# Kernel optimization log

Hardware: AMD Instinct MI355X
Metric: run time of the kernel (lower is better)

Reference implementation:

```python
import jax, jax.numpy as jnp
import numpy as np

N = 20000      # nodes
E = 320000     # edges (avg degree 16)
D_IN = 128     # input_dim
HID = 128      # graph_hidden_dim (per-head channels)
HEADS = 4


def setup_inputs() -> dict:
    key = jax.random.key(0)
    ks = jax.random.split(key, 16)
    def gl(k, shape, fan_in):
        return jax.random.normal(k, shape, jnp.float32) / np.float32(np.sqrt(fan_in))
    x = jax.random.normal(ks[0], (N, D_IN), jnp.float32)
    edge_index = jax.random.randint(ks[1], (2, E), 0, N, dtype=jnp.int64)
    # layer 0: in=D_IN, heads=4, concat -> 4*HID
    W0 = gl(ks[2], (D_IN, HEADS * HID), D_IN)
    a_src0 = gl(ks[3], (HEADS, HID), HID)
    a_dst0 = gl(ks[4], (HEADS, HID), HID)
    b0 = jnp.zeros((HEADS * HID,), jnp.float32)
    # layer 1: in=4*HID, heads=4, concat -> 4*HID
    W1 = gl(ks[5], (HEADS * HID, HEADS * HID), HEADS * HID)
    a_src1 = gl(ks[6], (HEADS, HID), HID)
    a_dst1 = gl(ks[7], (HEADS, HID), HID)
    b1 = jnp.zeros((HEADS * HID,), jnp.float32)
    # layer 2: in=4*HID, heads=1, no concat -> HID
    W2 = gl(ks[8], (HEADS * HID, HID), HEADS * HID)
    a_src2 = gl(ks[9], (1, HID), HID)
    a_dst2 = gl(ks[10], (1, HID), HID)
    b2 = jnp.zeros((HID,), jnp.float32)
    # output MLP: HID -> HID//2 -> 1
    Wm1 = gl(ks[11], (HID, HID // 2), HID)
    bm1 = jnp.zeros((HID // 2,), jnp.float32)
    Wm2 = gl(ks[12], (HID // 2, 1), HID // 2)
    bm2 = jnp.zeros((1,), jnp.float32)
    return dict(x=x, edge_index=edge_index, W0=W0, a_src0=a_src0, a_dst0=a_dst0, b0=b0,
                W1=W1, a_src1=a_src1, a_dst1=a_dst1, b1=b1,
                W2=W2, a_src2=a_src2, a_dst2=a_dst2, b2=b2,
                Wm1=Wm1, bm1=bm1, Wm2=Wm2, bm2=bm2)


def _gat(x, src, dst, W, a_s, a_d, b, heads, ch, concat):
    """PyG GATConv: per-head linear, edge attention with LeakyReLU(0.2),
    segment softmax over incoming edges, scatter-add aggregation."""
    n = x.shape[0]
    xl = (x @ W).reshape(n, heads, ch)                      # [N,H,C]
    a_src_n = jnp.einsum('nhc,hc->nh', xl, a_s)             # [N,H]
    a_dst_n = jnp.einsum('nhc,hc->nh', xl, a_d)
    e = jax.nn.leaky_relu(a_src_n[src] + a_dst_n[dst], 0.2) # [E,H]
    m = jax.ops.segment_max(e, dst, num_segments=n)
    ex = jnp.exp(e - m[dst])
    den = jax.ops.segment_sum(ex, dst, num_segments=n)
    alpha = ex / den[dst]                                   # self-loops keep den > 0
    out = jax.ops.segment_sum(alpha[:, :, None] * xl[src], dst, num_segments=n)  # [N,H,C]
    out = out.reshape(n, heads * ch) if concat else out.mean(axis=1)
    return out + b


def reference(x, edge_index, W0, a_src0, a_dst0, b0, W1, a_src1, a_dst1, b1,
              W2, a_src2, a_dst2, b2, Wm1, bm1, Wm2, bm2):
    n = x.shape[0]
    loops = jnp.arange(n, dtype=edge_index.dtype)           # add_self_loops (PyG default)
    src = jnp.concatenate([edge_index[0], loops])
    dst = jnp.concatenate([edge_index[1], loops])
    h = jax.nn.relu(_gat(x, src, dst, W0, a_src0, a_dst0, b0, HEADS, HID, True))
    h = jax.nn.relu(_gat(h, src, dst, W1, a_src1, a_dst1, b1, HEADS, HID, True))
    h = _gat(h, src, dst, W2, a_src2, a_dst2, b2, 1, HID, False)
    g = h.mean(axis=0, keepdims=True)                       # global mean pool, batch=None -> [1,HID]
    g = jax.nn.relu(g @ Wm1 + bm1)
    return g @ Wm2 + bm2                                    # predictions [1,1]
```

## Files before the change

kernel.cpp:

```cpp
#include <hip/hip_runtime.h>
#include <math.h>


typedef float f32x4 __attribute__((ext_vector_type(4)));
typedef float f32x2 __attribute__((ext_vector_type(2)));
typedef short s16x8 __attribute__((ext_vector_type(8)));
typedef short s16x4 __attribute__((ext_vector_type(4)));

__device__ inline ushort f2bf(float f) {
  unsigned u = __float_as_uint(f);
  u += 0x7FFF + ((u >> 16) & 1);
  return (ushort)(u >> 16);
}
__device__ inline float bf2f(ushort h) { return __uint_as_float((unsigned)h << 16); }
__device__ inline unsigned char f2fp8(float f) {
  int p = __builtin_amdgcn_cvt_pk_fp8_f32(f, f, 0, false);
  return (unsigned char)(p & 0xFF);
}

__global__ void prep_kernel(
    const float* __restrict__ W0, const float* __restrict__ W1,
    const float* __restrict__ W2, ushort* __restrict__ w0h, ushort* __restrict__ w0l,
    ushort* __restrict__ w1h, ushort* __restrict__ w1l, ushort* __restrict__ w2h,
    ushort* __restrict__ w2l, const int* __restrict__ ei, int* __restrict__ counts,
    int E, int n) {
  int idx = blockIdx.x * 256 + threadIdx.x;
  if (idx >= 98304) {
    int t = idx - 98304;
    if (t < E)          atomicAdd(&counts[ei[E + t]], 1);
    else if (t < E + n) atomicAdd(&counts[t - E], 1);
    return;
  }
  const float* W; ushort *th, *tl; int K, N;
  if (idx < 16384)      { W = W0; th = w0h; tl = w0l; K = 128; N = 512; }
  else if (idx < 81920) { idx -= 16384; W = W1; th = w1h; tl = w1l; K = 512; N = 512; }
  else                  { idx -= 81920; W = W2; th = w2h; tl = w2l; K = 512; N = 128; }
  int nn = idx % N;
  int k4 = (idx / N) << 2;
  s16x4 hv, lv;
#pragma unroll
  for (int r = 0; r < 4; ++r) {
    float w = W[(size_t)(k4 + r) * N + nn];
    ushort h = f2bf(w);
    hv[r] = (short)h;
    lv[r] = (short)f2bf(w - bf2f(h));
  }
  *(s16x4*)&th[(size_t)nn * K + k4] = hv;
  *(s16x4*)&tl[(size_t)nn * K + k4] = lv;
}

__global__ void scan1_kernel(const int* __restrict__ counts, int* __restrict__ partials,
                             int n) {
  __shared__ int sd[4];
  int i = blockIdx.x * 256 + threadIdx.x;
  int v = (i < n) ? counts[i] : 0;
  for (int m = 32; m; m >>= 1) v += __shfl_xor(v, m);
  if ((threadIdx.x & 63) == 0) sd[threadIdx.x >> 6] = v;
  __syncthreads();
  if (threadIdx.x == 0) partials[blockIdx.x] = sd[0] + sd[1] + sd[2] + sd[3];
}

__global__ void scan3_kernel(const int* __restrict__ counts, const int* __restrict__ partials,
                             int* __restrict__ offsets, int n) {
  __shared__ int sd[256];
  __shared__ int cw[4];
  __shared__ int carry_sh;
  int t = threadIdx.x;
  int pv = (t < blockIdx.x) ? partials[t] : 0;
  for (int m = 32; m; m >>= 1) pv += __shfl_xor(pv, m);
  if ((t & 63) == 0) cw[t >> 6] = pv;
  __syncthreads();
  if (t == 0) carry_sh = cw[0] + cw[1] + cw[2] + cw[3];
  int i = blockIdx.x * 256 + t;
  int v = (i < n) ? counts[i] : 0;
  sd[t] = v;
  __syncthreads();
  for (int off = 1; off < 256; off <<= 1) {
    int u = (t >= off) ? sd[t - off] : 0;
    __syncthreads();
    sd[t] += u;
    __syncthreads();
  }
  int carry = carry_sh;
  if (i < n) {
    offsets[i] = carry + sd[t] - v;
    if (i == n - 1) offsets[n] = carry + sd[t];
  }
}

__global__ void scatter_kernel(const int* __restrict__ ei, const int* __restrict__ offsets,
                               int* __restrict__ cursor, int* __restrict__ srcs,
                               int E, int n) {
  int t = blockIdx.x * blockDim.x + threadIdx.x;
  int s, d;
  if (t < E)          { s = ei[t]; d = ei[E + t]; }
  else if (t < E + n) { s = t - E; d = s; }
  else return;
  int pos = offsets[d] + atomicAdd(&cursor[d], 1);
  srcs[pos] = s;
}

template <int NC>
__device__ inline void gemm_epilogue(
    f32x4 (&acc)[2][4], unsigned char* __restrict__ Cb, const float* __restrict__ a_s,
    const float* __restrict__ a_d, float* __restrict__ asn, float* __restrict__ adn,
    float (*st_sh)[64][2], int M, int row0, int col0, int hidx,
    int tid, int lane, int wid, int wm, int wn, int fr) {
  constexpr int N = NC * 128;
  float asv[4], adv[4];
#pragma unroll
  for (int j = 0; j < 4; ++j) {
    asv[j] = a_s[hidx * 128 + wn + j * 16 + fr];
    adv[j] = a_d[hidx * 128 + wn + j * 16 + fr];
  }
  int rb = row0 + wm + ((lane >> 4) << 2);
  int cb = col0 + wn + fr;
#pragma unroll
  for (int i = 0; i < 2; ++i)
#pragma unroll
    for (int r = 0; r < 4; ++r) {
      int row = rb + i * 16 + r;
      float sp = 0.f, dp = 0.f;
#pragma unroll
      for (int j = 0; j < 4; ++j) {
        float c = acc[i][j][r];
        sp += c * asv[j];
        dp += c * adv[j];
        if (row < M) Cb[(size_t)row * N + cb + j * 16] = f2fp8(c);
      }
#pragma unroll
      for (int m = 1; m < 16; m <<= 1) {
        sp += __shfl_xor(sp, m);
        dp += __shfl_xor(dp, m);
      }
      if ((lane & 15) == 0) {
        int rowb = wm + i * 16 + ((lane >> 4) << 2) + r;
        st_sh[0][rowb][wid >> 1] = sp;
        st_sh[1][rowb][wid >> 1] = dp;
      }
    }
  __syncthreads();
  if (tid < 64) {
    int row = row0 + tid;
    if (row < M) {
      asn[(size_t)row * NC + hidx] = st_sh[0][tid][0] + st_sh[0][tid][1];
      adn[(size_t)row * NC + hidx] = st_sh[1][tid][0] + st_sh[1][tid][1];
    }
  }
}

template <int NC>
__global__ __launch_bounds__(256, 2) void gemm_f32a_kernel(
    const float* __restrict__ A, const ushort* __restrict__ Bth,
    const ushort* __restrict__ Btl, unsigned char* __restrict__ Cb,
    const float* __restrict__ a_s, const float* __restrict__ a_d,
    float* __restrict__ asn, float* __restrict__ adn,
    int M, int K) {
  __shared__ s16x8 Ash[4][64], Asl[4][64];
  __shared__ s16x8 Bsh[4][128], Bsl[4][128];
  __shared__ float st_sh[2][64][2];
  int id = blockIdx.x;
  int rs = (id / (8 * NC)) * 8 + (id & 7);
  int row0 = rs * 64;
  if (row0 >= M) return;
  int hidx = (id >> 3) % NC;
  int col0 = hidx * 128;
  int tid = threadIdx.x;
  int am = tid >> 2, aq = tid & 3;
  int bn = tid >> 1, bq = (tid & 1) << 1;
  int lane = tid & 63, wid = tid >> 6;
  int wm = (wid & 1) << 5, wn = (wid >> 1) << 6;
  int fr = lane & 15, fqq = lane >> 4;
  f32x4 acc[2][4] = {};
  const float* Arow = A + (size_t)(row0 + am) * K + aq * 8;
  bool avalid = (row0 + am) < M;
  const ushort* bhp = Bth + (size_t)(col0 + bn) * K + bq * 8;
  const ushort* blp = Btl + (size_t)(col0 + bn) * K + bq * 8;

  for (int k0 = 0; k0 < K; k0 += 32) {
    float v[8];
    if (avalid) {
      float4 t0 = *(const float4*)(Arow + k0);
      float4 t1 = *(const float4*)(Arow + k0 + 4);
      v[0] = t0.x; v[1] = t0.y; v[2] = t0.z; v[3] = t0.w;
      v[4] = t1.x; v[5] = t1.y; v[6] = t1.z; v[7] = t1.w;
    } else {
#pragma unroll
      for (int r = 0; r < 8; ++r) v[r] = 0.f;
    }
    s16x8 hv, lv;
#pragma unroll
    for (int r = 0; r < 8; ++r) {
      ushort h = f2bf(v[r]);
      hv[r] = (short)h;
      lv[r] = (short)f2bf(v[r] - bf2f(h));
    }
    Ash[aq][am] = hv;
    Asl[aq][am] = lv;
    Bsh[bq][bn]     = *(const s16x8*)(bhp + k0);
    Bsh[bq + 1][bn] = *(const s16x8*)(bhp + k0 + 8);
    Bsl[bq][bn]     = *(const s16x8*)(blp + k0);
    Bsl[bq + 1][bn] = *(const s16x8*)(blp + k0 + 8);
    __syncthreads();
    s16x8 ah[2], al[2], bh[4], bl[4];
#pragma unroll
    for (int i = 0; i < 2; ++i) {
      ah[i] = Ash[fqq][wm + i * 16 + fr];
      al[i] = Asl[fqq][wm + i * 16 + fr];
    }
#pragma unroll
    for (int j = 0; j < 4; ++j) {
      bh[j] = Bsh[fqq][wn + j * 16 + fr];
      bl[j] = Bsl[fqq][wn + j * 16 + fr];
    }
#pragma unroll
    for (int i = 0; i < 2; ++i)
#pragma unroll
      for (int j = 0; j < 4; ++j) {
        acc[i][j] = __builtin_amdgcn_mfma_f32_16x16x32_bf16(ah[i], bh[j], acc[i][j], 0, 0, 0);
        acc[i][j] = __builtin_amdgcn_mfma_f32_16x16x32_bf16(ah[i], bl[j], acc[i][j], 0, 0, 0);
        acc[i][j] = __builtin_amdgcn_mfma_f32_16x16x32_bf16(al[i], bh[j], acc[i][j], 0, 0, 0);
      }
    __syncthreads();
  }
  gemm_epilogue<NC>(acc, Cb, a_s, a_d, asn, adn, st_sh, M, row0, col0, hidx,
                    tid, lane, wid, wm, wn, fr);
}

template <int NC>
__global__ __launch_bounds__(256, 2) void gemm_bf16a_kernel(
    const ushort* __restrict__ A, const ushort* __restrict__ Bth,
    const ushort* __restrict__ Btl, unsigned char* __restrict__ Cb,
    const float* __restrict__ a_s, const float* __restrict__ a_d,
    float* __restrict__ asn, float* __restrict__ adn,
    int M, int K) {
  __shared__ s16x8 Ash[4][64];
  __shared__ s16x8 Bsh[4][128], Bsl[4][128];
  __shared__ float st_sh[2][64][2];
  int id = blockIdx.x;
  int rs = (id / (8 * NC)) * 8 + (id & 7);
  int row0 = rs * 64;
  if (row0 >= M) return;
  int hidx = (id >> 3) % NC;
  int col0 = hidx * 128;
  int tid = threadIdx.x;
  int am = tid >> 2, aq = tid & 3;
  int bn = tid >> 1, bq = (tid & 1) << 1;
  int lane = tid & 63, wid = tid >> 6;
  int wm = (wid & 1) << 5, wn = (wid >> 1) << 6;
  int fr = lane & 15, fqq = lane >> 4;
  f32x4 acc[2][4] = {};
  const ushort* Arow = A + (size_t)(row0 + am) * K + aq * 8;
  bool avalid = (row0 + am) < M;
  const ushort* bhp = Bth + (size_t)(col0 + bn) * K + bq * 8;
  const ushort* blp = Btl + (size_t)(col0 + bn) * K + bq * 8;
  const s16x8 zero8 = {};

  for (int k0 = 0; k0 < K; k0 += 32) {
    Ash[aq][am] = avalid ? *(const s16x8*)(Arow + k0) : zero8;
    Bsh[bq][bn]     = *(const s16x8*)(bhp + k0);
    Bsh[bq + 1][bn] = *(const s16x8*)(bhp + k0 + 8);
    Bsl[bq][bn]     = *(const s16x8*)(blp + k0);
    Bsl[bq + 1][bn] = *(const s16x8*)(blp + k0 + 8);
    __syncthreads();
    s16x8 ah[2], bh[4], bl[4];
#pragma unroll
    for (int i = 0; i < 2; ++i) ah[i] = Ash[fqq][wm + i * 16 + fr];
#pragma unroll
    for (int j = 0; j < 4; ++j) {
      bh[j] = Bsh[fqq][wn + j * 16 + fr];
      bl[j] = Bsl[fqq][wn + j * 16 + fr];
    }
#pragma unroll
    for (int i = 0; i < 2; ++i)
#pragma unroll
      for (int j = 0; j < 4; ++j) {
        acc[i][j] = __builtin_amdgcn_mfma_f32_16x16x32_bf16(ah[i], bh[j], acc[i][j], 0, 0, 0);
        acc[i][j] = __builtin_amdgcn_mfma_f32_16x16x32_bf16(ah[i], bl[j], acc[i][j], 0, 0, 0);
      }
    __syncthreads();
  }
  gemm_epilogue<NC>(acc, Cb, a_s, a_d, asn, adn, st_sh, M, row0, col0, hidx,
                    tid, lane, wid, wm, wn, fr);
}

template <int NC>
__global__ __launch_bounds__(256, 2) void gemm_bf16a128_kernel(
    const ushort* __restrict__ A, const ushort* __restrict__ Bth,
    const ushort* __restrict__ Btl, unsigned char* __restrict__ Cb,
    const float* __restrict__ a_s, const float* __restrict__ a_d,
    float* __restrict__ asn, float* __restrict__ adn,
    int M, int K) {
  constexpr int N = NC * 128;
  __shared__ s16x8 Ash[4][128];
  __shared__ s16x8 Bsh[4][128], Bsl[4][128];
  __shared__ float st_sh[2][128][2];
  int id = blockIdx.x;
  int rs = (id / (8 * NC)) * 8 + (id & 7);
  int row0 = rs * 128;
  if (row0 >= M) return;
  int hidx = (id >> 3) % NC;
  int col0 = hidx * 128;
  int tid = threadIdx.x;
  int am = tid >> 1, aq = (tid & 1) << 1;
  int bn = tid >> 1, bq = (tid & 1) << 1;
  int lane = tid & 63, wid = tid >> 6;
  int wm = (wid & 1) << 6, wn = (wid >> 1) << 6;
  int fr = lane & 15, fqq = lane >> 4;
  f32x4 acc[4][4] = {};
  const ushort* Arow = A + (size_t)(row0 + am) * K + aq * 8;
  bool avalid = (row0 + am) < M;
  const ushort* bhp = Bth + (size_t)(col0 + bn) * K + bq * 8;
  const ushort* blp = Btl + (size_t)(col0 + bn) * K + bq * 8;
  const s16x8 zero8 = {};

  for (int k0 = 0; k0 < K; k0 += 32) {
    Ash[aq][am]     = avalid ? *(const s16x8*)(Arow + k0) : zero8;
    Ash[aq + 1][am] = avalid ? *(const s16x8*)(Arow + k0 + 8) : zero8;
    Bsh[bq][bn]     = *(const s16x8*)(bhp + k0);
    Bsh[bq + 1][bn] = *(const s16x8*)(bhp + k0 + 8);
    Bsl[bq][bn]     = *(const s16x8*)(blp + k0);
    Bsl[bq + 1][bn] = *(const s16x8*)(blp + k0 + 8);
    __syncthreads();
    s16x8 ah[4], bh[4], bl[4];
#pragma unroll
    for (int i = 0; i < 4; ++i) ah[i] = Ash[fqq][wm + i * 16 + fr];
#pragma unroll
    for (int j = 0; j < 4; ++j) {
      bh[j] = Bsh[fqq][wn + j * 16 + fr];
      bl[j] = Bsl[fqq][wn + j * 16 + fr];
    }
#pragma unroll
    for (int i = 0; i < 4; ++i)
#pragma unroll
      for (int j = 0; j < 4; ++j) {
        acc[i][j] = __builtin_amdgcn_mfma_f32_16x16x32_bf16(ah[i], bh[j], acc[i][j], 0, 0, 0);
        acc[i][j] = __builtin_amdgcn_mfma_f32_16x16x32_bf16(ah[i], bl[j], acc[i][j], 0, 0, 0);
      }
    __syncthreads();
  }
  float asv[4], adv[4];
#pragma unroll
  for (int j = 0; j < 4; ++j) {
    asv[j] = a_s[hidx * 128 + wn + j * 16 + fr];
    adv[j] = a_d[hidx * 128 + wn + j * 16 + fr];
  }
  int rb = row0 + wm + ((lane >> 4) << 2);
  int cb = col0 + wn + fr;
#pragma unroll
  for (int i = 0; i < 4; ++i)
#pragma unroll
    for (int r = 0; r < 4; ++r) {
      int row = rb + i * 16 + r;
      float sp = 0.f, dp = 0.f;
#pragma unroll
      for (int j = 0; j < 4; ++j) {
        float c = acc[i][j][r];
        sp += c * asv[j];
        dp += c * adv[j];
        if (row < M) Cb[(size_t)row * N + cb + j * 16] = f2fp8(c);
      }
#pragma unroll
      for (int m = 1; m < 16; m <<= 1) {
        sp += __shfl_xor(sp, m);
        dp += __shfl_xor(dp, m);
      }
      if ((lane & 15) == 0) {
        int rowb = wm + i * 16 + ((lane >> 4) << 2) + r;
        st_sh[0][rowb][wid >> 1] = sp;
        st_sh[1][rowb][wid >> 1] = dp;
      }
    }
  __syncthreads();
  if (tid < 128) {
    int row = row0 + tid;
    if (row < M) {
      asn[(size_t)row * NC + hidx] = st_sh[0][tid][0] + st_sh[0][tid][1];
      adn[(size_t)row * NC + hidx] = st_sh[1][tid][0] + st_sh[1][tid][1];
    }
  }
}

__global__ __launch_bounds__(256) void agg4_kernel(
    const unsigned char* __restrict__ xl, const float* __restrict__ asn,
    const float* __restrict__ adn, const int* __restrict__ offsets,
    const int* __restrict__ srcs, const float* __restrict__ bias,
    ushort* __restrict__ out, int n) {
  __shared__ float alpha_sh[4][4][64];
  __shared__ int src_sh[4][64];
  int wib = threadIdx.x >> 6, lane = threadIdx.x & 63;
  int nd = blockIdx.x * 4 + wib;
  if (nd >= n) return;
  int beg = offsets[nd], deg = offsets[nd + 1] - beg;
  float4 adl = *(const float4*)&adn[(size_t)nd * 4];
  int ch0 = lane << 3;
  int hm = lane >> 4;
  float den[4] = {0.f, 0.f, 0.f, 0.f};
  float acc[8] = {};

  for (int j0 = 0; j0 < deg; j0 += 64) {
    int j = j0 + lane;
    int s = 0;
    float w0 = 0.f, w1 = 0.f, w2 = 0.f, w3 = 0.f;
    if (j < deg) {
      s = srcs[beg + j];
      float4 av = *(const float4*)&asn[(size_t)s * 4];
      float e;
      e = av.x + adl.x; e = (e > 0.f) ? e : 0.2f * e; w0 = __expf(fminf(e, 30.f));
      e = av.y + adl.y; e = (e > 0.f) ? e : 0.2f * e; w1 = __expf(fminf(e, 30.f));
      e = av.z + adl.z; e = (e > 0.f) ? e : 0.2f * e; w2 = __expf(fminf(e, 30.f));
      e = av.w + adl.w; e = (e > 0.f) ? e : 0.2f * e; w3 = __expf(fminf(e, 30.f));
      den[0] += w0; den[1] += w1; den[2] += w2; den[3] += w3;
    }
    src_sh[wib][lane] = s;
    alpha_sh[wib][0][lane] = w0;
    alpha_sh[wib][1][lane] = w1;
    alpha_sh[wib][2][lane] = w2;
    alpha_sh[wib][3][lane] = w3;
    __builtin_amdgcn_wave_barrier();
    int cl = min(64, deg - j0);
    int jj = 0;
    for (; jj + 8 <= cl; jj += 8) {
      int4 sv0 = *(const int4*)&src_sh[wib][jj];
      int4 sv1 = *(const int4*)&src_sh[wib][jj + 4];
      float4 av0 = *(const float4*)&alpha_sh[wib][hm][jj];
      float4 av1 = *(const float4*)&alpha_sh[wib][hm][jj + 4];
      uint2 v[8];
      v[0] = *(const uint2*)(xl + (size_t)sv0.x * 512 + ch0);
      v[1] = *(const uint2*)(xl + (size_t)sv0.y * 512 + ch0);
      v[2] = *(const uint2*)(xl + (size_t)sv0.z * 512 + ch0);
      v[3] = *(const uint2*)(xl + (size_t)sv0.w * 512 + ch0);
      v[4] = *(const uint2*)(xl + (size_t)sv1.x * 512 + ch0);
      v[5] = *(const uint2*)(xl + (size_t)sv1.y * 512 + ch0);
      v[6] = *(const uint2*)(xl + (size_t)sv1.z * 512 + ch0);
      v[7] = *(const uint2*)(xl + (size_t)sv1.w * 512 + ch0);
      float a[8] = {av0.x, av0.y, av0.z, av0.w, av1.x, av1.y, av1.z, av1.w};
#pragma unroll
      for (int u = 0; u < 8; ++u) {
        f32x2 c01 = __builtin_amdgcn_cvt_pk_f32_fp8((int)v[u].x, false);
        f32x2 c23 = __builtin_amdgcn_cvt_pk_f32_fp8((int)v[u].x, true);
        f32x2 c45 = __builtin_amdgcn_cvt_pk_f32_fp8((int)v[u].y, false);
        f32x2 c67 = __builtin_amdgcn_cvt_pk_f32_fp8((int)v[u].y, true);
        acc[0] += a[u] * c01[0]; acc[1] += a[u] * c01[1];
        acc[2] += a[u] * c23[0]; acc[3] += a[u] * c23[1];
        acc[4] += a[u] * c45[0]; acc[5] += a[u] * c45[1];
        acc[6] += a[u] * c67[0]; acc[7] += a[u] * c67[1];
      }
    }
    for (; jj < cl; ++jj) {
      int s2 = src_sh[wib][jj];
      float a = alpha_sh[wib][hm][jj];
      uint2 v = *(const uint2*)(xl + (size_t)s2 * 512 + ch0);
      f32x2 c01 = __builtin_amdgcn_cvt_pk_f32_fp8((int)v.x, false);
      f32x2 c23 = __builtin_amdgcn_cvt_pk_f32_fp8((int)v.x, true);
      f32x2 c45 = __builtin_amdgcn_cvt_pk_f32_fp8((int)v.y, false);
      f32x2 c67 = __builtin_amdgcn_cvt_pk_f32_fp8((int)v.y, true);
      acc[0] += a * c01[0]; acc[1] += a * c01[1];
      acc[2] += a * c23[0]; acc[3] += a * c23[1];
      acc[4] += a * c45[0]; acc[5] += a * c45[1];
      acc[6] += a * c67[0]; acc[7] += a * c67[1];
    }
    __builtin_amdgcn_wave_barrier();
  }
#pragma unroll
  for (int h = 0; h < 4; ++h)
    for (int m = 1; m < 64; m <<= 1) den[h] += __shfl_xor(den[h], m);
  float d = (hm == 0) ? den[0] : (hm == 1) ? den[1] : (hm == 2) ? den[2] : den[3];
  float inv = 1.f / d;
  s16x8 ob;
#pragma unroll
  for (int i = 0; i < 8; ++i)
    ob[i] = (short)f2bf(fmaxf(acc[i] * inv + bias[ch0 + i], 0.f));
  *(s16x8*)(out + (size_t)nd * 512 + ch0) = ob;
}

__global__ __launch_bounds__(256) void agg1_pool_kernel(
    const unsigned char* __restrict__ xl, const float* __restrict__ asn,
    const float* __restrict__ adn, const int* __restrict__ offsets,
    const int* __restrict__ srcs, const float* __restrict__ bias,
    float* __restrict__ g_part, int n) {
  __shared__ float alpha_sh[4][64];
  __shared__ int src_sh[4][64];
  __shared__ float red_sh[4][128];
  int wib = threadIdx.x >> 6, lane = threadIdx.x & 63;
  int nd = blockIdx.x * 4 + wib;
  bool valid = nd < n;
  int ch0 = lane << 1;
  float acc0 = 0.f, acc1 = 0.f;

  if (valid) {
    int beg = offsets[nd], deg = offsets[nd + 1] - beg;
    float adl = adn[nd];
    float den = 0.f;
    for (int j0 = 0; j0 < deg; j0 += 64) {
      int j = j0 + lane;
      int s = 0;
      float w = 0.f;
      if (j < deg) {
        s = srcs[beg + j];
        float e = asn[s] + adl;
        e = (e > 0.f) ? e : 0.2f * e;
        w = __expf(fminf(e, 30.f));
        den += w;
      }
      src_sh[wib][lane] = s;
      alpha_sh[wib][lane] = w;
      __builtin_amdgcn_wave_barrier();
      int cl = min(64, deg - j0);
      int jj = 0;
      for (; jj + 4 <= cl; jj += 4) {
        int4 sv = *(const int4*)&src_sh[wib][jj];
        float4 av = *(const float4*)&alpha_sh[wib][jj];
        uint v0 = *(const ushort*)(xl + (size_t)sv.x * 128 + ch0);
        uint v1 = *(const ushort*)(xl + (size_t)sv.y * 128 + ch0);
        uint v2 = *(const ushort*)(xl + (size_t)sv.z * 128 + ch0);
        uint v3 = *(const ushort*)(xl + (size_t)sv.w * 128 + ch0);
        f32x2 c0 = __builtin_amdgcn_cvt_pk_f32_fp8((int)v0, false);
        f32x2 c1 = __builtin_amdgcn_cvt_pk_f32_fp8((int)v1, false);
        f32x2 c2 = __builtin_amdgcn_cvt_pk_f32_fp8((int)v2, false);
        f32x2 c3 = __builtin_amdgcn_cvt_pk_f32_fp8((int)v3, false);
        acc0 += av.x * c0[0]; acc1 += av.x * c0[1];
        acc0 += av.y * c1[0]; acc1 += av.y * c1[1];
        acc0 += av.z * c2[0]; acc1 += av.z * c2[1];
        acc0 += av.w * c3[0]; acc1 += av.w * c3[1];
      }
      for (; jj < cl; ++jj) {
        int s2 = src_sh[wib][jj];
        float a = alpha_sh[wib][jj];
        uint v = *(const ushort*)(xl + (size_t)s2 * 128 + ch0);
        f32x2 c = __builtin_amdgcn_cvt_pk_f32_fp8((int)v, false);
        acc0 += a * c[0]; acc1 += a * c[1];
      }
      __builtin_amdgcn_wave_barrier();
    }
    for (int m = 1; m < 64; m <<= 1) den += __shfl_xor(den, m);
    float inv = 1.f / den;
    acc0 = acc0 * inv + bias[ch0 + 0];
    acc1 = acc1 * inv + bias[ch0 + 1];
  }
  red_sh[wib][ch0] = acc0;
  red_sh[wib][ch0 + 1] = acc1;
  __syncthreads();
  if (threadIdx.x < 128) {
    float s = red_sh[0][threadIdx.x] + red_sh[1][threadIdx.x] +
              red_sh[2][threadIdx.x] + red_sh[3][threadIdx.x];
    atomicAdd(&g_part[(blockIdx.x & 63) * 128 + threadIdx.x], s);
  }
}

__global__ void mlp_kernel(const float* __restrict__ g_part,
                           const float* __restrict__ Wm1, const float* __restrict__ bm1,
                           const float* __restrict__ Wm2, const float* __restrict__ bm2,
                           float* __restrict__ out, float invn) {
  __shared__ float gs[128];
  __shared__ float hs[64];
  int t = threadIdx.x;
  float s = 0.f;
  for (int k = 0; k < 64; ++k) s += g_part[k * 128 + t];
  gs[t] = s * invn;
  __syncthreads();
  if (t < 64) {
    float acc = bm1[t];
    for (int c = 0; c < 128; ++c) acc += gs[c] * Wm1[c * 64 + t];
    hs[t] = fmaxf(acc, 0.f);
  }
  __syncthreads();
  if (t == 0) {
    float o = bm2[0];
    for (int j = 0; j < 64; ++j) o += hs[j] * Wm2[j];
    out[0] = o;
  }
}

extern "C" void kernel_launch(void* const* d_in, const int* in_sizes, int n_in,
                              void* d_out, int out_size, void* d_ws, size_t ws_size,
                              hipStream_t stream) {
  const float* x   = (const float*)d_in[0];
  const int*   ei  = (const int*)d_in[1];
  const float* W0  = (const float*)d_in[2];
  const float* as0 = (const float*)d_in[3];
  const float* ad0 = (const float*)d_in[4];
  const float* b0  = (const float*)d_in[5];
  const float* W1  = (const float*)d_in[6];
  const float* as1 = (const float*)d_in[7];
  const float* ad1 = (const float*)d_in[8];
  const float* b1  = (const float*)d_in[9];
  const float* W2  = (const float*)d_in[10];
  const float* as2 = (const float*)d_in[11];
  const float* ad2 = (const float*)d_in[12];
  const float* b2  = (const float*)d_in[13];
  const float* Wm1 = (const float*)d_in[14];
  const float* bm1 = (const float*)d_in[15];
  const float* Wm2 = (const float*)d_in[16];
  const float* bm2 = (const float*)d_in[17];

  const int N = in_sizes[0] / 128;
  const int E = in_sizes[1] / 2;
  const int ET = E + N;

  ushort* hb  = (ushort*)d_ws;
  unsigned char* xlb = (unsigned char*)(hb + (size_t)N * 512);
  float*  asn = (float*)(xlb + (size_t)N * 512);
  float*  adn = asn + (size_t)N * 4;
  float*  gp  = adn + (size_t)N * 4;
  int* counts = (int*)(gp + 64 * 128);
  int* cursor = counts + N;
  int* offs   = cursor + N;
  int* srcs   = offs + N + 1;
  int* parts  = srcs + ET;
  ushort* w0h = (ushort*)(((uintptr_t)(parts + 1024) + 63) & ~(uintptr_t)63);
  ushort* w0l = w0h + 512 * 128;
  ushort* w1h = w0l + 512 * 128;
  ushort* w1l = w1h + 512 * 512;
  ushort* w2h = w1l + 512 * 512;
  ushort* w2l = w2h + 128 * 512;

  hipMemsetAsync(gp, 0, (size_t)(64 * 128 + 2 * N) * sizeof(int), stream);

  prep_kernel<<<(98304 + ET + 255) / 256, 256, 0, stream>>>(
      W0, W1, W2, w0h, w0l, w1h, w1l, w2h, w2l, ei, counts, E, N);

  int ebl = (ET + 255) / 256;
  int nb = (N + 255) / 256;
  scan1_kernel<<<nb, 256, 0, stream>>>(counts, parts, N);
  scan3_kernel<<<nb, 256, 0, stream>>>(counts, parts, offs, N);
  scatter_kernel<<<ebl, 256, 0, stream>>>(ei, offs, cursor, srcs, E, N);

  int nwb4 = (N + 3) / 4;
  int rsn = (N + 63) / 64;
  int rsp = ((rsn + 7) / 8) * 8;
  int blk0 = rsp * 4;
  int rs128 = (N + 127) / 128;
  int rsp128 = ((rs128 + 7) / 8) * 8;
  int blk1 = rsp128 * 4;
  int blk2 = rsp;

  gemm_f32a_kernel<4><<<blk0, 256, 0, stream>>>(x, w0h, w0l, xlb, as0, ad0,
                                                asn, adn, N, 128);
  agg4_kernel<<<nwb4, 256, 0, stream>>>(xlb, asn, adn, offs, srcs, b0, hb, N);

  gemm_bf16a128_kernel<4><<<blk1, 256, 0, stream>>>(hb, w1h, w1l, xlb, as1, ad1,
                                                    asn, adn, N, 512);
  agg4_kernel<<<nwb4, 256, 0, stream>>>(xlb, asn, adn, offs, srcs, b1, hb, N);

  gemm_bf16a_kernel<1><<<blk2, 256, 0, stream>>>(hb, w2h, w2l, xlb, as2, ad2,
                                                 asn, adn, N, 512);
  agg1_pool_kernel<<<nwb4, 256, 0, stream>>>(xlb, asn, adn, offs, srcs, b2, gp, N);

  mlp_kernel<<<1, 128, 0, stream>>>(gp, Wm1, bm1, Wm2, bm2, (float*)d_out,
                                    1.0f / (float)N);
}
```

Measured before the change: 280.2 us.

## Fuse all pipeline stages into one cooperative persistent kernel with grid syncs

Replaces the sequence of separate launches (memset, prep, scan, scatter, three GEMMs, three aggregations, MLP) with one cooperative persistent kernel. Each stage loops over virtual block ids and is separated from the next by grid.sync(), with shared memory held in a union sized for the largest stage. This removes per-launch overhead and inter-kernel gaps. In exchange it adds grid-wide barrier costs, a launch bound of 3 blocks per CU that may limit registers for the GEMMs, and load imbalance where a stage has fewer blocks than the grid; the old multi-kernel path is kept as a fallback.

```diff
diff --git a/kernel.cpp b/kernel.cpp
--- a/kernel.cpp
+++ b/kernel.cpp
@@ -1,5 +1,8 @@
 #include <hip/hip_runtime.h>
+#include <hip/hip_cooperative_groups.h>
 #include <math.h>
+
+namespace cg = cooperative_groups;
 
 
 typedef float f32x4 __attribute__((ext_vector_type(4)));
@@ -18,13 +21,21 @@
   return (unsigned char)(p & 0xFF);
 }
 
-__global__ void prep_kernel(
-    const float* __restrict__ W0, const float* __restrict__ W1,
+struct SG0 { s16x8 Ash[4][64]; s16x8 Asl[4][64]; s16x8 Bsh[4][128]; s16x8 Bsl[4][128]; float st[2][64][2]; };
+struct SG1 { s16x8 Ash[4][128]; s16x8 Bsh[4][128]; s16x8 Bsl[4][128]; float st[2][128][2]; };
+struct SG2 { s16x8 Ash[4][64]; s16x8 Bsh[4][128]; s16x8 Bsl[4][128]; float st[2][64][2]; };
+struct SA4 { float alpha[4][4][64]; int src[4][64]; };
+struct SA1 { float alpha[4][64]; int src[4][64]; float red[4][128]; };
+struct SSCAN { int sd[256]; int cw[4]; int carry; };
+struct SMLP { float gs[128]; float hs[64]; };
+union SMem { SG0 g0; SG1 g1; SG2 g2; SA4 a4; SA1 a1; SSCAN scan; SMLP mlp; };
+
+__device__ inline void prep_item(
+    int idx, const float* __restrict__ W0, const float* __restrict__ W1,
     const float* __restrict__ W2, ushort* __restrict__ w0h, ushort* __restrict__ w0l,
     ushort* __restrict__ w1h, ushort* __restrict__ w1l, ushort* __restrict__ w2h,
     ushort* __restrict__ w2l, const int* __restrict__ ei, int* __restrict__ counts,
     int E, int n) {
-  int idx = blockIdx.x * 256 + threadIdx.x;
   if (idx >= 98304) {
     int t = idx - 98304;
     if (t < E)          atomicAdd(&counts[ei[E + t]], 1);
@@ -49,49 +60,49 @@
   *(s16x4*)&tl[(size_t)nn * K + k4] = lv;
 }
 
-__global__ void scan1_kernel(const int* __restrict__ counts, int* __restrict__ partials,
-                             int n) {
-  __shared__ int sd[4];
-  int i = blockIdx.x * 256 + threadIdx.x;
+__device__ inline void scan1_body(int vb, const int* __restrict__ counts,
+                                  int* __restrict__ partials, int n, SSCAN& s) {
+  int t = threadIdx.x;
+  int i = vb * 256 + t;
   int v = (i < n) ? counts[i] : 0;
   for (int m = 32; m; m >>= 1) v += __shfl_xor(v, m);
-  if ((threadIdx.x & 63) == 0) sd[threadIdx.x >> 6] = v;
-  __syncthreads();
-  if (threadIdx.x == 0) partials[blockIdx.x] = sd[0] + sd[1] + sd[2] + sd[3];
-}
-
-__global__ void scan3_kernel(const int* __restrict__ counts, const int* __restrict__ partials,
-                             int* __restrict__ offsets, int n) {
-  __shared__ int sd[256];
-  __shared__ int cw[4];
-  __shared__ int carry_sh;
+  if ((t & 63) == 0) s.cw[t >> 6] = v;
+  __syncthreads();
+  if (t == 0) partials[vb] = s.cw[0] + s.cw[1] + s.cw[2] + s.cw[3];
+  __syncthreads();
+}
+
+__device__ inline void scan3_body(int vb, const int* __restrict__ counts,
+                                  const int* __restrict__ partials,
+                                  int* __restrict__ offsets, int n, SSCAN& s) {
   int t = threadIdx.x;
-  int pv = (t < blockIdx.x) ? partials[t] : 0;
+  int pv = (t < vb) ? partials[t] : 0;
   for (int m = 32; m; m >>= 1) pv += __shfl_xor(pv, m);
-  if ((t & 63) == 0) cw[t >> 6] = pv;
-  __syncthreads();
-  if (t == 0) carry_sh = cw[0] + cw[1] + cw[2] + cw[3];
-  int i = blockIdx.x * 256 + t;
+  if ((t & 63) == 0) s.cw[t >> 6] = pv;
+  __syncthreads();
+  if (t == 0) s.carry = s.cw[0] + s.cw[1] + s.cw[2] + s.cw[3];
+  int i = vb * 256 + t;
   int v = (i < n) ? counts[i] : 0;
-  sd[t] = v;
+  s.sd[t] = v;
   __syncthreads();
   for (int off = 1; off < 256; off <<= 1) {
-    int u = (t >= off) ? sd[t - off] : 0;
+    int u = (t >= off) ? s.sd[t - off] : 0;
     __syncthreads();
-    sd[t] += u;
+    s.sd[t] += u;
     __syncthreads();
   }
-  int carry = carry_sh;
+  int carry = s.carry;
   if (i < n) {
-    offsets[i] = carry + sd[t] - v;
-    if (i == n - 1) offsets[n] = carry + sd[t];
-  }
-}
-
-__global__ void scatter_kernel(const int* __restrict__ ei, const int* __restrict__ offsets,
-                               int* __restrict__ cursor, int* __restrict__ srcs,
-                               int E, int n) {
-  int t = blockIdx.x * blockDim.x + threadIdx.x;
+    offsets[i] = carry + s.sd[t] - v;
+    if (i == n - 1) offsets[n] = carry + s.sd[t];
+  }
+  __syncthreads();
+}
+
+__device__ inline void scatter_item(int t, const int* __restrict__ ei,
+                                    const int* __restrict__ offsets,
+                                    int* __restrict__ cursor, int* __restrict__ srcs,
+                                    int E, int n) {
   int s, d;
   if (t < E)          { s = ei[t]; d = ei[E + t]; }
   else if (t < E + n) { s = t - E; d = s; }
@@ -150,16 +161,11 @@
 }
 
 template <int NC>
-__global__ __launch_bounds__(256, 2) void gemm_f32a_kernel(
-    const float* __restrict__ A, const ushort* __restrict__ Bth,
+__device__ inline void gemm_f32a_body(
+    int id, const float* __restrict__ A, const ushort* __restrict__ Bth,
     const ushort* __restrict__ Btl, unsigned char* __restrict__ Cb,
     const float* __restrict__ a_s, const float* __restrict__ a_d,
-    float* __restrict__ asn, float* __restrict__ adn,
-    int M, int K) {
-  __shared__ s16x8 Ash[4][64], Asl[4][64];
-  __shared__ s16x8 Bsh[4][128], Bsl[4][128];
-  __shared__ float st_sh[2][64][2];
-  int id = blockIdx.x;
+    float* __restrict__ asn, float* __restrict__ adn, int M, int K, SG0& sm) {
   int rs = (id / (8 * NC)) * 8 + (id & 7);
   int row0 = rs * 64;
   if (row0 >= M) return;
@@ -195,23 +201,23 @@
       hv[r] = (short)h;
       lv[r] = (short)f2bf(v[r] - bf2f(h));
     }
-    Ash[aq][am] = hv;
-    Asl[aq][am] = lv;
-    Bsh[bq][bn]     = *(const s16x8*)(bhp + k0);
-    Bsh[bq + 1][bn] = *(const s16x8*)(bhp + k0 + 8);
-    Bsl[bq][bn]     = *(const s16x8*)(blp + k0);
-    Bsl[bq + 1][bn] = *(const s16x8*)(blp + k0 + 8);
+    sm.Ash[aq][am] = hv;
+    sm.Asl[aq][am] = lv;
+    sm.Bsh[bq][bn]     = *(const s16x8*)(bhp + k0);
+    sm.Bsh[bq + 1][bn] = *(const s16x8*)(bhp + k0 + 8);
+    sm.Bsl[bq][bn]     = *(const s16x8*)(blp + k0);
+    sm.Bsl[bq + 1][bn] = *(const s16x8*)(blp + k0 + 8);
     __syncthreads();
     s16x8 ah[2], al[2], bh[4], bl[4];
 #pragma unroll
     for (int i = 0; i < 2; ++i) {
-      ah[i] = Ash[fqq][wm + i * 16 + fr];
-      al[i] = Asl[fqq][wm + i * 16 + fr];
+      ah[i] = sm.Ash[fqq][wm + i * 16 + fr];
+      al[i] = sm.Asl[fqq][wm + i * 16 + fr];
     }
 #pragma unroll
     for (int j = 0; j < 4; ++j) {
-      bh[j] = Bsh[fqq][wn + j * 16 + fr];
-      bl[j] = Bsl[fqq][wn + j * 16 + fr];
+      bh[j] = sm.Bsh[fqq][wn + j * 16 + fr];
+      bl[j] = sm.Bsl[fqq][wn + j * 16 + fr];
     }
 #pragma unroll
     for (int i = 0; i < 2; ++i)
@@ -223,21 +229,16 @@
       }
     __syncthreads();
   }
-  gemm_epilogue<NC>(acc, Cb, a_s, a_d, asn, adn, st_sh, M, row0, col0, hidx,
+  gemm_epilogue<NC>(acc, Cb, a_s, a_d, asn, adn, sm.st, M, row0, col0, hidx,
                     tid, lane, wid, wm, wn, fr);
 }
 
 template <int NC>
-__global__ __launch_bounds__(256, 2) void gemm_bf16a_kernel(
-    const ushort* __restrict__ A, const ushort* __restrict__ Bth,
+__device__ inline void gemm_bf16a_body(
+    int id, const ushort* __restrict__ A, const ushort* __restrict__ Bth,
     const ushort* __restrict__ Btl, unsigned char* __restrict__ Cb,
     const float* __restrict__ a_s, const float* __restrict__ a_d,
-    float* __restrict__ asn, float* __restrict__ adn,
-    int M, int K) {
-  __shared__ s16x8 Ash[4][64];
-  __shared__ s16x8 Bsh[4][128], Bsl[4][128];
-  __shared__ float st_sh[2][64][2];
-  int id = blockIdx.x;
+    float* __restrict__ asn, float* __restrict__ adn, int M, int K, SG2& sm) {
   int rs = (id / (8 * NC)) * 8 + (id & 7);
   int row0 = rs * 64;
   if (row0 >= M) return;
@@ -257,19 +258,19 @@
   const s16x8 zero8 = {};
 
   for (int k0 = 0; k0 < K; k0 += 32) {
-    Ash[aq][am] = avalid ? *(const s16x8*)(Arow + k0) : zero8;
-    Bsh[bq][bn]     = *(const s16x8*)(bhp + k0);
-    Bsh[bq + 1][bn] = *(const s16x8*)(bhp + k0 + 8);
-    Bsl[bq][bn]     = *(const s16x8*)(blp + k0);
-    Bsl[bq + 1][bn] = *(const s16x8*)(blp + k0 + 8);
+    sm.Ash[aq][am] = avalid ? *(const s16x8*)(Arow + k0) : zero8;
+    sm.Bsh[bq][bn]     = *(const s16x8*)(bhp + k0);
+    sm.Bsh[bq + 1][bn] = *(const s16x8*)(bhp + k0 + 8);
+    sm.Bsl[bq][bn]     = *(const s16x8*)(blp + k0);
+    sm.Bsl[bq + 1][bn] = *(const s16x8*)(blp + k0 + 8);
     __syncthreads();
     s16x8 ah[2], bh[4], bl[4];
 #pragma unroll
-    for (int i = 0; i < 2; ++i) ah[i] = Ash[fqq][wm + i * 16 + fr];
+    for (int i = 0; i < 2; ++i) ah[i] = sm.Ash[fqq][wm + i * 16 + fr];
 #pragma unroll
     for (int j = 0; j < 4; ++j) {
-      bh[j] = Bsh[fqq][wn + j * 16 + fr];
-      bl[j] = Bsl[fqq][wn + j * 16 + fr];
+      bh[j] = sm.Bsh[fqq][wn + j * 16 + fr];
+      bl[j] = sm.Bsl[fqq][wn + j * 16 + fr];
     }
 #pragma unroll
     for (int i = 0; i < 2; ++i)
@@ -280,22 +281,17 @@
       }
     __syncthreads();
   }
-  gemm_epilogue<NC>(acc, Cb, a_s, a_d, asn, adn, st_sh, M, row0, col0, hidx,
+  gemm_epilogue<NC>(acc, Cb, a_s, a_d, asn, adn, sm.st, M, row0, col0, hidx,
                     tid, lane, wid, wm, wn, fr);
 }
 
 template <int NC>
-__global__ __launch_bounds__(256, 2) void gemm_bf16a128_kernel(
-    const ushort* __restrict__ A, const ushort* __restrict__ Bth,
+__device__ inline void gemm_bf16a128_body(
+    int id, const ushort* __restrict__ A, const ushort* __restrict__ Bth,
     const ushort* __restrict__ Btl, unsigned char* __restrict__ Cb,
     const float* __restrict__ a_s, const float* __restrict__ a_d,
-    float* __restrict__ asn, float* __restrict__ adn,
-    int M, int K) {
+    float* __restrict__ asn, float* __restrict__ adn, int M, int K, SG1& sm) {
   constexpr int N = NC * 128;
-  __shared__ s16x8 Ash[4][128];
-  __shared__ s16x8 Bsh[4][128], Bsl[4][128];
-  __shared__ float st_sh[2][128][2];
-  int id = blockIdx.x;
   int rs = (id / (8 * NC)) * 8 + (id & 7);
   int row0 = rs * 128;
   if (row0 >= M) return;
@@ -315,20 +311,20 @@
   const s16x8 zero8 = {};
 
   for (int k0 = 0; k0 < K; k0 += 32) {
-    Ash[aq][am]     = avalid ? *(const s16x8*)(Arow + k0) : zero8;
-    Ash[aq + 1][am] = avalid ? *(const s16x8*)(Arow + k0 + 8) : zero8;
-    Bsh[bq][bn]     = *(const s16x8*)(bhp + k0);
-    Bsh[bq + 1][bn] = *(const s16x8*)(bhp + k0 + 8);
-    Bsl[bq][bn]     = *(const s16x8*)(blp + k0);
-    Bsl[bq + 1][bn] = *(const s16x8*)(blp + k0 + 8);
+    sm.Ash[aq][am]     = avalid ? *(const s16x8*)(Arow + k0) : zero8;
+    sm.Ash[aq + 1][am] = avalid ? *(const s16x8*)(Arow + k0 + 8) : zero8;
+    sm.Bsh[bq][bn]     = *(const s16x8*)(bhp + k0);
+    sm.Bsh[bq + 1][bn] = *(const s16x8*)(bhp + k0 + 8);
+    sm.Bsl[bq][bn]     = *(const s16x8*)(blp + k0);
+    sm.Bsl[bq + 1][bn] = *(const s16x8*)(blp + k0 + 8);
     __syncthreads();
     s16x8 ah[4], bh[4], bl[4];
 #pragma unroll
-    for (int i = 0; i < 4; ++i) ah[i] = Ash[fqq][wm + i * 16 + fr];
+    for (int i = 0; i < 4; ++i) ah[i] = sm.Ash[fqq][wm + i * 16 + fr];
 #pragma unroll
     for (int j = 0; j < 4; ++j) {
-      bh[j] = Bsh[fqq][wn + j * 16 + fr];
-      bl[j] = Bsl[fqq][wn + j * 16 + fr];
+      bh[j] = sm.Bsh[fqq][wn + j * 16 + fr];
+      bl[j] = sm.Bsl[fqq][wn + j * 16 + fr];
     }
 #pragma unroll
     for (int i = 0; i < 4; ++i)
@@ -367,29 +363,27 @@
       }
       if ((lane & 15) == 0) {
         int rowb = wm + i * 16 + ((lane >> 4) << 2) + r;
-        st_sh[0][rowb][wid >> 1] = sp;
-        st_sh[1][rowb][wid >> 1] = dp;
+        sm.st[0][rowb][wid >> 1] = sp;
+        sm.st[1][rowb][wid >> 1] = dp;
       }
     }
   __syncthreads();
   if (tid < 128) {
     int row = row0 + tid;
     if (row < M) {
-      asn[(size_t)row * NC + hidx] = st_sh[0][tid][0] + st_sh[0][tid][1];
-      adn[(size_t)row * NC + hidx] = st_sh[1][tid][0] + st_sh[1][tid][1];
-    }
-  }
-}
-
-__global__ __launch_bounds__(256) void agg4_kernel(
-    const unsigned char* __restrict__ xl, const float* __restrict__ asn,
+      asn[(size_t)row * NC + hidx] = sm.st[0][tid][0] + sm.st[0][tid][1];
+      adn[(size_t)row * NC + hidx] = sm.st[1][tid][0] + sm.st[1][tid][1];
+    }
+  }
+}
+
+__device__ inline void agg4_body(
+    int vb, const unsigned char* __restrict__ xl, const float* __restrict__ asn,
     const float* __restrict__ adn, const int* __restrict__ offsets,
     const int* __restrict__ srcs, const float* __restrict__ bias,
-    ushort* __restrict__ out, int n) {
-  __shared__ float alpha_sh[4][4][64];
-  __shared__ int src_sh[4][64];
+    ushort* __restrict__ out, int n, SA4& sm) {
   int wib = threadIdx.x >> 6, lane = threadIdx.x & 63;
-  int nd = blockIdx.x * 4 + wib;
+  int nd = vb * 4 + wib;
   if (nd >= n) return;
   int beg = offsets[nd], deg = offsets[nd + 1] - beg;
   float4 adl = *(const float4*)&adn[(size_t)nd * 4];
@@ -412,19 +406,19 @@
       e = av.w + adl.w; e = (e > 0.f) ? e : 0.2f * e; w3 = __expf(fminf(e, 30.f));
       den[0] += w0; den[1] += w1; den[2] += w2; den[3] += w3;
     }
-    src_sh[wib][lane] = s;
-    alpha_sh[wib][0][lane] = w0;
-    alpha_sh[wib][1][lane] = w1;
-    alpha_sh[wib][2][lane] = w2;
-    alpha_sh[wib][3][lane] = w3;
+    sm.src[wib][lane] = s;
+    sm.alpha[wib][0][lane] = w0;
+    sm.alpha[wib][1][lane] = w1;
+    sm.alpha[wib][2][lane] = w2;
+    sm.alpha[wib][3][lane] = w3;
     __builtin_amdgcn_wave_barrier();
     int cl = min(64, deg - j0);
     int jj = 0;
     for (; jj + 8 <= cl; jj += 8) {
-      int4 sv0 = *(const int4*)&src_sh[wib][jj];
-      int4 sv1 = *(const int4*)&src_sh[wib][jj + 4];
-      float4 av0 = *(const float4*)&alpha_sh[wib][hm][jj];
-      float4 av1 = *(const float4*)&alpha_sh[wib][hm][jj + 4];
+      int4 sv0 = *(const int4*)&sm.src[wib][jj];
+      int4 sv1 = *(const int4*)&sm.src[wib][jj + 4];
+      float4 av0 = *(const float4*)&sm.alpha[wib][hm][jj];
+      float4 av1 = *(const float4*)&sm.alpha[wib][hm][jj + 4];
       uint2 v[8];
       v[0] = *(const uint2*)(xl + (size_t)sv0.x * 512 + ch0);
       v[1] = *(const uint2*)(xl + (size_t)sv0.y * 512 + ch0);
@@ -448,8 +442,8 @@
       }
     }
     for (; jj < cl; ++jj) {
-      int s2 = src_sh[wib][jj];
-      float a = alpha_sh[wib][hm][jj];
+      int s2 = sm.src[wib][jj];
+      float a = sm.alpha[wib][hm][jj];
       uint2 v = *(const uint2*)(xl + (size_t)s2 * 512 + ch0);
       f32x2 c01 = __builtin_amdgcn_cvt_pk_f32_fp8((int)v.x, false);
       f32x2 c23 = __builtin_amdgcn_cvt_pk_f32_fp8((int)v.x, true);
@@ -474,16 +468,13 @@
   *(s16x8*)(out + (size_t)nd * 512 + ch0) = ob;
 }
 
-__global__ __launch_bounds__(256) void agg1_pool_kernel(
-    const unsigned char* __restrict__ xl, const float* __restrict__ asn,
+__device__ inline void agg1_body(
+    int vb, const unsigned char* __restrict__ xl, const float* __restrict__ asn,
     const float* __restrict__ adn, const int* __restrict__ offsets,
     const int* __restrict__ srcs, const float* __restrict__ bias,
-    float* __restrict__ g_part, int n) {
-  __shared__ float alpha_sh[4][64];
-  __shared__ int src_sh[4][64];
-  __shared__ float red_sh[4][128];
+    float* __restrict__ g_part, int n, SA1& sm) {
   int wib = threadIdx.x >> 6, lane = threadIdx.x & 63;
-  int nd = blockIdx.x * 4 + wib;
+  int nd = vb * 4 + wib;
   bool valid = nd < n;
   int ch0 = lane << 1;
   float acc0 = 0.f, acc1 = 0.f;
@@ -503,14 +494,14 @@
         w = __expf(fminf(e, 30.f));
         den += w;
       }
-      src_sh[wib][lane] = s;
-      alpha_sh[wib][lane] = w;
+      sm.src[wib][lane] = s;
+      sm.alpha[wib][lane] = w;
       __builtin_amdgcn_wave_barrier();
       int cl = min(64, deg - j0);
       int jj = 0;
       for (; jj + 4 <= cl; jj += 4) {
-        int4 sv = *(const int4*)&src_sh[wib][jj];
-        float4 av = *(const float4*)&alpha_sh[wib][jj];
+        int4 sv = *(const int4*)&sm.src[wib][jj];
+        float4 av = *(const float4*)&sm.alpha[wib][jj];
         uint v0 = *(const ushort*)(xl + (size_t)sv.x * 128 + ch0);
         uint v1 = *(const ushort*)(xl + (size_t)sv.y * 128 + ch0);
         uint v2 = *(const ushort*)(xl + (size_t)sv.z * 128 + ch0);
@@ -525,8 +516,8 @@
         acc0 += av.w * c3[0]; acc1 += av.w * c3[1];
       }
       for (; jj < cl; ++jj) {
-        int s2 = src_sh[wib][jj];
-        float a = alpha_sh[wib][jj];
+        int s2 = sm.src[wib][jj];
+        float a = sm.alpha[wib][jj];
         uint v = *(const ushort*)(xl + (size_t)s2 * 128 + ch0);
         f32x2 c = __builtin_amdgcn_cvt_pk_f32_fp8((int)v, false);
         acc0 += a * c[0]; acc1 += a * c[1];
@@ -538,38 +529,202 @@
     acc0 = acc0 * inv + bias[ch0 + 0];
     acc1 = acc1 * inv + bias[ch0 + 1];
   }
-  red_sh[wib][ch0] = acc0;
-  red_sh[wib][ch0 + 1] = acc1;
+  sm.red[wib][ch0] = acc0;
+  sm.red[wib][ch0 + 1] = acc1;
   __syncthreads();
   if (threadIdx.x < 128) {
-    float s = red_sh[0][threadIdx.x] + red_sh[1][threadIdx.x] +
-              red_sh[2][threadIdx.x] + red_sh[3][threadIdx.x];
-    atomicAdd(&g_part[(blockIdx.x & 63) * 128 + threadIdx.x], s);
-  }
+    float s = sm.red[0][threadIdx.x] + sm.red[1][threadIdx.x] +
+              sm.red[2][threadIdx.x] + sm.red[3][threadIdx.x];
+    atomicAdd(&g_part[(vb & 63) * 128 + threadIdx.x], s);
+  }
+  __syncthreads();
+}
+
+__device__ inline void mlp_body(const float* __restrict__ g_part,
+                                const float* __restrict__ Wm1, const float* __restrict__ bm1,
+                                const float* __restrict__ Wm2, const float* __restrict__ bm2,
+                                float* __restrict__ out, float invn, SMLP& sm) {
+  int t = threadIdx.x;
+  if (t < 128) {
+    float s = 0.f;
+    for (int k = 0; k < 64; ++k) s += g_part[k * 128 + t];
+    sm.gs[t] = s * invn;
+  }
+  __syncthreads();
+  if (t < 64) {
+    float acc = bm1[t];
+    for (int c = 0; c < 128; ++c) acc += sm.gs[c] * Wm1[c * 64 + t];
+    sm.hs[t] = fmaxf(acc, 0.f);
+  }
+  __syncthreads();
+  if (t == 0) {
+    float o = bm2[0];
+    for (int j = 0; j < 64; ++j) o += sm.hs[j] * Wm2[j];
+    out[0] = o;
+  }
+}
+
+struct KParams {
+  const float* x; const int* ei;
+  const float* W0; const float* as0; const float* ad0; const float* b0;
+  const float* W1; const float* as1; const float* ad1; const float* b1;
+  const float* W2; const float* as2; const float* ad2; const float* b2;
+  const float* Wm1; const float* bm1; const float* Wm2; const float* bm2;
+  ushort* w0h; ushort* w0l; ushort* w1h; ushort* w1l; ushort* w2h; ushort* w2l;
+  ushort* hb; unsigned char* xlb; float* asn; float* adn; float* gp;
+  int* counts; int* cursor; int* offs; int* srcs; int* parts;
+  float* out; int N; int E;
+};
+
+__global__ __launch_bounds__(256, 3) void mega_kernel(KParams p) {
+  __shared__ SMem sm;
+  cg::grid_group grid = cg::this_grid();
+  const int n = p.N, E = p.E, ET = E + n;
+  const int tid = threadIdx.x;
+  const int gsz = gridDim.x;
+  const int nthr = gsz * 256;
+  const int gidx = blockIdx.x * 256 + tid;
+
+  {
+    int total = 64 * 128 + 2 * n;
+    int* z = (int*)p.gp;
+    for (int i = gidx; i < total; i += nthr) z[i] = 0;
+  }
+  grid.sync();
+
+  {
+    int total = 98304 + ET;
+    for (int i = gidx; i < total; i += nthr)
+      prep_item(i, p.W0, p.W1, p.W2, p.w0h, p.w0l, p.w1h, p.w1l, p.w2h, p.w2l,
+                p.ei, p.counts, E, n);
+  }
+  grid.sync();
+
+  const int nb = (n + 255) >> 8;
+  for (int vb = blockIdx.x; vb < nb; vb += gsz) scan1_body(vb, p.counts, p.parts, n, sm.scan);
+  grid.sync();
+  for (int vb = blockIdx.x; vb < nb; vb += gsz) scan3_body(vb, p.counts, p.parts, p.offs, n, sm.scan);
+  grid.sync();
+  for (int i = gidx; i < ET; i += nthr) scatter_item(i, p.ei, p.offs, p.cursor, p.srcs, E, n);
+  grid.sync();
+
+  const int rsn = (n + 63) >> 6, rsp = (rsn + 7) & ~7;
+  const int rs128 = (n + 127) >> 7, rsp128 = (rs128 + 7) & ~7;
+  const int nwb4 = (n + 3) >> 2;
+
+  {
+    int blk0 = rsp * 4;
+    for (int id = blockIdx.x; id < blk0; id += gsz)
+      gemm_f32a_body<4>(id, p.x, p.w0h, p.w0l, p.xlb, p.as0, p.ad0, p.asn, p.adn,
+                        n, 128, sm.g0);
+  }
+  grid.sync();
+  for (int vb = blockIdx.x; vb < nwb4; vb += gsz)
+    agg4_body(vb, p.xlb, p.asn, p.adn, p.offs, p.srcs, p.b0, p.hb, n, sm.a4);
+  grid.sync();
+  {
+    int blk1 = rsp128 * 4;
+    for (int id = blockIdx.x; id < blk1; id += gsz)
+      gemm_bf16a128_body<4>(id, p.hb, p.w1h, p.w1l, p.xlb, p.as1, p.ad1, p.asn, p.adn,
+                            n, 512, sm.g1);
+  }
+  grid.sync();
+  for (int vb = blockIdx.x; vb < nwb4; vb += gsz)
+    agg4_body(vb, p.xlb, p.asn, p.adn, p.offs, p.srcs, p.b1, p.hb, n, sm.a4);
+  grid.sync();
+  for (int id = blockIdx.x; id < rsp; id += gsz)
+    gemm_bf16a_body<1>(id, p.hb, p.w2h, p.w2l, p.xlb, p.as2, p.ad2, p.asn, p.adn,
+                       n, 512, sm.g2);
+  grid.sync();
+  for (int vb = blockIdx.x; vb < nwb4; vb += gsz)
+    agg1_body(vb, p.xlb, p.asn, p.adn, p.offs, p.srcs, p.b2, p.gp, n, sm.a1);
+  grid.sync();
+  if (blockIdx.x == 0)
+    mlp_body(p.gp, p.Wm1, p.bm1, p.Wm2, p.bm2, p.out, 1.0f / (float)n, sm.mlp);
+}
+
+__global__ void prep_kernel(
+    const float* __restrict__ W0, const float* __restrict__ W1,
+    const float* __restrict__ W2, ushort* __restrict__ w0h, ushort* __restrict__ w0l,
+    ushort* __restrict__ w1h, ushort* __restrict__ w1l, ushort* __restrict__ w2h,
+    ushort* __restrict__ w2l, const int* __restrict__ ei, int* __restrict__ counts,
+    int E, int n) {
+  prep_item(blockIdx.x * 256 + threadIdx.x, W0, W1, W2, w0h, w0l, w1h, w1l, w2h, w2l,
+            ei, counts, E, n);
+}
+
+__global__ void scan1_kernel(const int* __restrict__ counts, int* __restrict__ partials,
+                             int n) {
+  __shared__ SSCAN s;
+  scan1_body(blockIdx.x, counts, partials, n, s);
+}
+
+__global__ void scan3_kernel(const int* __restrict__ counts, const int* __restrict__ partials,
+                             int* __restrict__ offsets, int n) {
+  __shared__ SSCAN s;
+  scan3_body(blockIdx.x, counts, partials, offsets, n, s);
+}
+
+__global__ void scatter_kernel(const int* __restrict__ ei, const int* __restrict__ offsets,
+                               int* __restrict__ cursor, int* __restrict__ srcs,
+                               int E, int n) {
+  scatter_item(blockIdx.x * blockDim.x + threadIdx.x, ei, offsets, cursor, srcs, E, n);
+}
+
+template <int NC>
+__global__ __launch_bounds__(256, 2) void gemm_f32a_kernel(
+    const float* __restrict__ A, const ushort* __restrict__ Bth,
+    const ushort* __restrict__ Btl, unsigned char* __restrict__ Cb,
+    const float* __restrict__ a_s, const float* __restrict__ a_d,
+    float* __restrict__ asn, float* __restrict__ adn, int M, int K) {
+  __shared__ SG0 s;
+  gemm_f32a_body<NC>(blockIdx.x, A, Bth, Btl, Cb, a_s, a_d, asn, adn, M, K, s);
+}
+
+template <int NC>
+__global__ __launch_bounds__(256, 2) void gemm_bf16a_kernel(
+    const ushort* __restrict__ A, const ushort* __restrict__ Bth,
+    const ushort* __restrict__ Btl, unsigned char* __restrict__ Cb,
+    const float* __restrict__ a_s, const float* __restrict__ a_d,
+    float* __restrict__ asn, float* __restrict__ adn, int M, int K) {
+  __shared__ SG2 s;
+  gemm_bf16a_body<NC>(blockIdx.x, A, Bth, Btl, Cb, a_s, a_d, asn, adn, M, K, s);
+}
+
+template <int NC>
+__global__ __launch_bounds__(256, 2) void gemm_bf16a128_kernel(
+    const ushort* __restrict__ A, const ushort* __restrict__ Bth,
+    const ushort* __restrict__ Btl, unsigned char* __restrict__ Cb,
+    const float* __restrict__ a_s, const float* __restrict__ a_d,
+    float* __restrict__ asn, float* __restrict__ adn, int M, int K) {
+  __shared__ SG1 s;
+  gemm_bf16a128_body<NC>(blockIdx.x, A, Bth, Btl, Cb, a_s, a_d, asn, adn, M, K, s);
+}
+
+__global__ __launch_bounds__(256) void agg4_kernel(
+    const unsigned char* __restrict__ xl, const float* __restrict__ asn,
+    const float* __restrict__ adn, const int* __restrict__ offsets,
+    const int* __restrict__ srcs, const float* __restrict__ bias,
+    ushort* __restrict__ out, int n) {
+  __shared__ SA4 s;
+  agg4_body(blockIdx.x, xl, asn, adn, offsets, srcs, bias, out, n, s);
+}
+
+__global__ __launch_bounds__(256) void agg1_pool_kernel(
+    const unsigned char* __restrict__ xl, const float* __restrict__ asn,
+    const float* __restrict__ adn, const int* __restrict__ offsets,
+    const int* __restrict__ srcs, const float* __restrict__ bias,
+    float* __restrict__ g_part, int n) {
+  __shared__ SA1 s;
+  agg1_body(blockIdx.x, xl, asn, adn, offsets, srcs, bias, g_part, n, s);
 }
 
 __global__ void mlp_kernel(const float* __restrict__ g_part,
                            const float* __restrict__ Wm1, const float* __restrict__ bm1,
                            const float* __restrict__ Wm2, const float* __restrict__ bm2,
                            float* __restrict__ out, float invn) {
-  __shared__ float gs[128];
-  __shared__ float hs[64];
-  int t = threadIdx.x;
-  float s = 0.f;
-  for (int k = 0; k < 64; ++k) s += g_part[k * 128 + t];
-  gs[t] = s * invn;
-  __syncthreads();
-  if (t < 64) {
-    float acc = bm1[t];
-    for (int c = 0; c < 128; ++c) acc += gs[c] * Wm1[c * 64 + t];
-    hs[t] = fmaxf(acc, 0.f);
-  }
-  __syncthreads();
-  if (t == 0) {
-    float o = bm2[0];
-    for (int j = 0; j < 64; ++j) o += hs[j] * Wm2[j];
-    out[0] = o;
-  }
+  __shared__ SMLP s;
+  mlp_body(g_part, Wm1, bm1, Wm2, bm2, out, invn, s);
 }
 
 extern "C" void kernel_launch(void* const* d_in, const int* in_sizes, int n_in,
@@ -615,6 +770,37 @@
   ushort* w2h = w1l + 512 * 512;
   ushort* w2l = w2h + 128 * 512;
 
+  static int nblk = 0;
+  if (nblk == 0) {
+    int dev = 0;
+    hipGetDevice(&dev);
+    hipDeviceProp_t prop;
+    int occ = 0;
+    if (hipGetDeviceProperties(&prop, dev) == hipSuccess &&
+        hipOccupancyMaxActiveBlocksPerMultiprocessor(&occ, mega_kernel, 256, 0) ==
+            hipSuccess && occ > 0)
+      nblk = prop.multiProcessorCount * occ;
+    if (nblk <= 0) nblk = -1;
+  }
+
+  hipError_t cerr = hipErrorUnknown;
+  if (nblk > 0) {
+    KParams kp;
+    kp.x = x; kp.ei = ei;
+    kp.W0 = W0; kp.as0 = as0; kp.ad0 = ad0; kp.b0 = b0;
+    kp.W1 = W1; kp.as1 = as1; kp.ad1 = ad1; kp.b1 = b1;
+    kp.W2 = W2; kp.as2 = as2; kp.ad2 = ad2; kp.b2 = b2;
+    kp.Wm1 = Wm1; kp.bm1 = bm1; kp.Wm2 = Wm2; kp.bm2 = bm2;
+    kp.w0h = w0h; kp.w0l = w0l; kp.w1h = w1h; kp.w1l = w1l; kp.w2h = w2h; kp.w2l = w2l;
+    kp.hb = hb; kp.xlb = xlb; kp.asn = asn; kp.adn = adn; kp.gp = gp;
+    kp.counts = counts; kp.cursor = cursor; kp.offs = offs; kp.srcs = srcs;
+    kp.parts = parts; kp.out = (float*)d_out; kp.N = N; kp.E = E;
+    void* kargs[] = {(void*)&kp};
+    cerr = hipLaunchCooperativeKernel(mega_kernel, dim3(nblk), dim3(256), kargs, 0,
+                                      stream);
+  }
+  if (cerr == hipSuccess) return;
+
   hipMemsetAsync(gp, 0, (size_t)(64 * 128 + 2 * N) * sizeof(int), stream);
 
   prep_kernel<<<(98304 + ET + 255) / 256, 256, 0, stream>>>(
```

Result: slower. 822.0 us (+193.4%).
